# Optimization experiments

Measured on AMD Instinct MI355X. Metric: run time of the kernel, lower is better.

## Reference

```python
import jax, jax.numpy as jnp
import numpy as np
from jax import lax

NUM_CLASSES = 80
TOPK = 13
ALPHA = 1.0
BETA = 6.0
EPS = 1e-9
P = 150000
N = 256


def _make_boxes(key, n, scale):
    k1, k2 = jax.random.split(key)
    xy = jax.random.uniform(k1, (n, 2), dtype=jnp.float32) * scale
    wh = jax.random.uniform(k2, (n, 2), dtype=jnp.float32) * (0.2 * scale) + 1.0
    return jnp.concatenate([xy, xy + wh], axis=-1)  # valid x1y1x2y2


def setup_inputs() -> dict:
    key = jax.random.key(0)
    k1, k2, k3, k4 = jax.random.split(key, 4)
    cls_pred = jax.random.uniform(k1, (P, NUM_CLASSES), dtype=jnp.float32)
    bbox_pred = _make_boxes(k2, P, 640.0)
    bbox_gt = _make_boxes(k3, N, 640.0)
    # FG labels are > 0 (code indexes cls_pred[label-1])
    label_gt = jax.random.randint(k4, (N, 1), 1, NUM_CLASSES + 1, dtype=jnp.int32)
    return {"cls_pred": cls_pred, "bbox_pred": bbox_pred, "label_gt": label_gt, "bbox_gt": bbox_gt}


def _ious(bbox1, bbox2, eps=EPS):
    # bbox1: (N,4) gt, bbox2: (P,4) pred -> (N,P)
    b1 = bbox1[:, None, :]
    b2 = bbox2[None, :, :]
    x1y1 = jnp.maximum(b1[..., 0:2], b2[..., 0:2])
    x2y2 = jnp.minimum(b1[..., 2:4], b2[..., 2:4])
    inter = jnp.clip(x2y2 - x1y1, 0.0).prod(-1)
    area1 = jnp.clip(b1[..., 2:4] - b1[..., 0:2], 0.0).prod(-1)
    area2 = jnp.clip(b2[..., 2:4] - b2[..., 0:2], 0.0).prod(-1)
    return inter / (area1 + area2 - inter + eps)


def _metrics_topk(metrics, topk, eps=EPS):
    n, num_priors = metrics.shape
    topk_vals, topk_idxs = lax.top_k(metrics, topk)  # (N,k)
    keep = topk_vals.max(axis=-1, keepdims=True) > eps
    topk_idxs = jnp.where(keep, topk_idxs, 0)
    rows = jnp.arange(n)[:, None]
    counts = jnp.zeros((n, num_priors), jnp.int32).at[rows, topk_idxs].add(1)
    is_in_topk = jnp.where(counts > 1, 0, counts)
    return is_in_topk.astype(metrics.dtype)


def reference(cls_pred, bbox_pred, label_gt, bbox_gt):
    num_priors, num_classes = cls_pred.shape
    n_gt = bbox_gt.shape[0]
    ious = _ious(bbox_gt, bbox_pred)  # (N,P)
    lbl = label_gt.reshape(-1).astype(jnp.int32)  # (N,)
    bbox_cls_scores = jnp.take(cls_pred.T, lbl - 1, axis=0)  # (N,P)
    alignment_metrics = jnp.power(bbox_cls_scores, ALPHA) * jnp.power(ious, BETA)
    mask_positive = _metrics_topk(alignment_metrics, TOPK)  # (N,P) float 0/1
    mask_positive_sum = mask_positive.sum(axis=0)  # (P,)
    # conflict resolution: priors claimed by >1 gt go to the max-iou gt.
    # Applying unconditionally equals the torch data-dependent branch.
    is_max_iou = (jnp.arange(n_gt)[:, None] == ious.argmax(axis=0)[None, :]).astype(ious.dtype)
    mask_positive = jnp.where(mask_positive_sum[None, :] > 1, is_max_iou, mask_positive)
    mask_positive_sum = mask_positive.sum(axis=0)
    assigned_gt_index = mask_positive.argmax(axis=0)  # (P,)
    assigned_labels = lbl[assigned_gt_index]  # (P,)
    assigned_cls = jax.nn.one_hot(assigned_labels - 1, num_classes, dtype=jnp.int32)
    assigned_bboxes = bbox_gt[assigned_gt_index]  # (P,4)
    assigned_labels = jnp.where(mask_positive_sum > 0, assigned_labels, 0)
    return (assigned_gt_index, assigned_labels, assigned_cls, assigned_bboxes)
```

## Files before the change

### kernel.cpp

```cpp
#include <hip/hip_runtime.h>

#define TOPK 13
#define NCLS 80
#define EPSF 1e-9f
#define NSEG 32
#define GPB  8
#define CAP3 512
#define SEGK 16

typedef unsigned long long u64;

__device__ __forceinline__ u64 shfl_xor64(u64 x, int m) {
    int lo = __shfl_xor((int)(unsigned)(x & 0xFFFFFFFFull), m, 64);
    int hi = __shfl_xor((int)(unsigned)(x >> 32), m, 64);
    return ((u64)(unsigned)hi << 32) | (unsigned)lo;
}

__global__ __launch_bounds__(256) void setup(const int* __restrict__ lbl,
                                             int* __restrict__ count,
                                             int* __restrict__ firstg,
                                             int* __restrict__ gorder, int P, int N) {
    int t = threadIdx.x;
    if (blockIdx.x == 0) {
        __shared__ int key[256];
        key[t] = (t < N) ? ((lbl[t] << 8) | t) : 0x7FFFFFFF;
        __syncthreads();
        for (int k = 2; k <= 256; k <<= 1) {
            for (int j = k >> 1; j >= 1; j >>= 1) {
                int ixj = t ^ j;
                if (ixj > t) {
                    int a = key[t], b = key[ixj];
                    bool up = ((t & k) == 0);
                    if (up ? (a > b) : (a < b)) { key[t] = b; key[ixj] = a; }
                }
                __syncthreads();
            }
        }
        if (t < N) gorder[t] = key[t] & 0xFF;
    } else {
        int base = (blockIdx.x - 1) * 1024 + t * 4;
        if (base + 3 < P) {
            *(int4*)&count[base]  = make_int4(0, 0, 0, 0);
            *(int4*)&firstg[base] = make_int4(0x7FFFFFFF, 0x7FFFFFFF, 0x7FFFFFFF, 0x7FFFFFFF);
        } else {
            for (int i = base; i < P; i++) { count[i] = 0; firstg[i] = 0x7FFFFFFF; }
        }
    }
}

__global__ __launch_bounds__(512, 8) void phaseA1(const float* __restrict__ cls,
                                                  const float4* __restrict__ bboxp,
                                                  const float4* __restrict__ bboxg,
                                                  const int* __restrict__ lbl,
                                                  const int* __restrict__ gorder,
                                                  u64* __restrict__ cand,
                                                  int P, int N, int seglen) {
#pragma clang fp contract(off)
    const int s = blockIdx.x, tile = blockIdx.y, t = threadIdx.x;
    const int wv = t >> 6, lane = t & 63;
    const int pstart = s * seglen;
    int pend = pstart + seglen; if (pend > P) pend = P;

    __shared__ int pbuf[GPB][CAP3];
    __shared__ int ctr[GPB];

    float4 gb[GPB];
#pragma unroll
    for (int j = 0; j < GPB; j++) {
        int gi8 = tile * GPB + j;
        int gj = (gi8 < N) ? gorder[gi8] : -1;
        gb[j] = (gj >= 0) ? bboxg[gj] : make_float4(0.f, 0.f, 0.f, 0.f);
    }
    if (t < GPB) ctr[t] = 0;
    __syncthreads();

    auto testapp = [&](float4 pb, int p, bool force) {
#pragma unroll
        for (int j = 0; j < GPB; j++) {
            float dx = fminf(gb[j].z, pb.z) - fmaxf(gb[j].x, pb.x);
            float dy = fminf(gb[j].w, pb.w) - fmaxf(gb[j].y, pb.y);
            bool want = ((dx > 0.0f) && (dy > 0.0f)) || force;
            if (want) {
                int slot = atomicAdd(&ctr[j], 1);
                if (slot < CAP3) pbuf[j][slot] = p;
            }
        }
    };

    int p = pstart + t;
    if (p < pend) { testapp(bboxp[p], p, t < 16); p += 512; }
    for (; p + 1536 < pend; p += 2048) {
        float4 pb0 = bboxp[p];
        float4 pb1 = bboxp[p + 512];
        float4 pb2 = bboxp[p + 1024];
        float4 pb3 = bboxp[p + 1536];
        testapp(pb0, p, false);
        testapp(pb1, p + 512, false);
        testapp(pb2, p + 1024, false);
        testapp(pb3, p + 1536, false);
    }
    for (; p < pend; p += 512) testapp(bboxp[p], p, false);
    __syncthreads();

    if (wv >= GPB / 2) return;

    const int half = lane >> 5;
    const int l    = lane & 31;
    const int slot = (wv << 1) | half;
    const int gi8 = tile * GPB + slot;
    const bool myValid = gi8 < N;
    const int gj = myValid ? gorder[gi8] : 0;
    const float4 gbw = bboxg[gj];
    const float gaw = fmaxf(gbw.z - gbw.x, 0.0f) * fmaxf(gbw.w - gbw.y, 0.0f);
    const int cidx = lbl[gj] - 1;
    const int rawtotal = ctr[slot];

    u64 K[16];
#pragma unroll
    for (int k = 0; k < 16; k++) K[k] = 0ull;

    auto ins = [&](u64 key) {
        if (key > K[TOPK - 1]) {
#pragma unroll
            for (int k = TOPK - 1; k >= 1; k--) {
                bool a = key > K[k - 1];
                K[k] = a ? K[k - 1] : (key > K[k] ? key : K[k]);
            }
            if (key > K[0]) K[0] = key;
        }
    };

    auto evalk = [&](float4 pb, float sc, int pp) -> u64 {
        float pa = fmaxf(pb.z - pb.x, 0.0f) * fmaxf(pb.w - pb.y, 0.0f);
        float xx1 = fmaxf(gbw.x, pb.x), yy1 = fmaxf(gbw.y, pb.y);
        float xx2 = fminf(gbw.z, pb.z), yy2 = fminf(gbw.w, pb.w);
        float inter = fmaxf(xx2 - xx1, 0.0f) * fmaxf(yy2 - yy1, 0.0f);
        float iou = inter / (((gaw + pa) - inter) + EPSF);
        float i2 = iou * iou;
        float m = sc * ((i2 * i2) * i2);
        unsigned ub = __float_as_uint(m);
        ub ^= ((unsigned)((int)ub >> 31)) | 0x80000000u;
        return ((u64)ub << 32) | (unsigned)(0x7FFFFFFF - pp);
    };

    if (rawtotal <= CAP3) {
        int e = l;
        for (; e + 32 < rawtotal; e += 64) {
            int pp0 = pbuf[slot][e];
            int pp1 = pbuf[slot][e + 32];
            float4 pb0 = bboxp[pp0];
            float4 pb1 = bboxp[pp1];
            float sc0 = cls[(size_t)pp0 * NCLS + cidx];
            float sc1 = cls[(size_t)pp1 * NCLS + cidx];
            u64 k0 = evalk(pb0, sc0, pp0);
            u64 k1 = evalk(pb1, sc1, pp1);
            ins(k0);
            ins(k1);
        }
        for (; e < rawtotal; e += 32) {
            int pp = pbuf[slot][e];
            float4 pb = bboxp[pp];
            float sc = cls[(size_t)pp * NCLS + cidx];
            ins(evalk(pb, sc, pp));
        }
    } else if (myValid) {
        for (int pp = pstart + l; pp < pend; pp += 32) {
            float4 pb = bboxp[pp];
            float sc = cls[(size_t)pp * NCLS + cidx];
            ins(evalk(pb, sc, pp));
        }
    }

    for (int str = 1; str <= 16; str <<= 1) {
#pragma unroll
        for (int i = 0; i < 8; i++) {
            u64 pa = shfl_xor64(K[15 - i], str);
            u64 pb = shfl_xor64(K[i], str);
            u64 a = K[i], b = K[15 - i];
            K[i]      = (a > pa) ? a : pa;
            K[15 - i] = (b > pb) ? b : pb;
        }
        if (str == 16) break;
#pragma unroll
        for (int j = 8; j >= 1; j >>= 1) {
#pragma unroll
            for (int i = 0; i < 16; i++) {
                if ((i & j) == 0) {
                    u64 a = K[i], b = K[i | j];
                    K[i] = (a > b) ? a : b;
                    K[i | j] = (a > b) ? b : a;
                }
            }
        }
    }

    u64 outk = 0ull;
#pragma unroll
    for (int k = 0; k < SEGK; k++) outk = (l == k) ? K[k] : outk;
    if (l < SEGK && myValid)
        cand[((size_t)gj * NSEG + s) * SEGK + l] = outk;
}

__global__ __launch_bounds__(64) void phaseA2(const u64* __restrict__ cand,
                                              int* __restrict__ count,
                                              int* __restrict__ firstg) {
    const int g = blockIdx.x;
    const int lane = threadIdx.x;
    const u64* src = cand + (size_t)g * (NSEG * SEGK);

    u64 K[16];
#pragma unroll
    for (int k = 0; k < 16; k++) K[k] = 0ull;

#pragma unroll
    for (int k = 0; k < (NSEG * SEGK) / 64; k++) {
        u64 key = src[lane + (k << 6)];
        if (key > K[TOPK - 1]) {
#pragma unroll
            for (int q = TOPK - 1; q >= 1; q--) {
                bool a = key > K[q - 1];
                K[q] = a ? K[q - 1] : (key > K[q] ? key : K[q]);
            }
            if (key > K[0]) K[0] = key;
        }
    }

    for (int str = 1; str < 64; str <<= 1) {
#pragma unroll
        for (int i = 0; i < 8; i++) {
            u64 pa = shfl_xor64(K[15 - i], str);
            u64 pb = shfl_xor64(K[i], str);
            u64 a = K[i], b = K[15 - i];
            K[i]      = (a > pa) ? a : pa;
            K[15 - i] = (b > pb) ? b : pb;
        }
#pragma unroll
        for (int j = 8; j >= 1; j >>= 1) {
#pragma unroll
            for (int i = 0; i < 16; i++) {
                if ((i & j) == 0) {
                    u64 a = K[i], b = K[i | j];
                    K[i] = (a > b) ? a : b;
                    K[i | j] = (a > b) ? b : a;
                }
            }
        }
    }

    const unsigned encEpsHi = __float_as_uint(EPSF) | 0x80000000u;
    if (lane < TOPK && (unsigned)(K[0] >> 32) > encEpsHi) {
        u64 outk = 0ull;
#pragma unroll
        for (int k = 0; k < TOPK; k++) outk = (lane == k) ? K[k] : outk;
        int pi = 0x7FFFFFFF - (int)(unsigned)(outk & 0xFFFFFFFFull);
        atomicAdd(&count[pi], 1);
        atomicMin(&firstg[pi], g);
    }
}

__global__ __launch_bounds__(256) void phaseCF(const float4* __restrict__ bboxp,
                                               const float4* __restrict__ bboxg,
                                               const int* __restrict__ lbl,
                                               const int* __restrict__ count,
                                               const int* __restrict__ firstg,
                                               float* __restrict__ out0,
                                               float* __restrict__ out1,
                                               float4* __restrict__ outcls4,
                                               float4* __restrict__ outbox4, int P, int N) {
#pragma clang fp contract(off)
    __shared__ float4 gbS[256];
    __shared__ int glS[256];
    __shared__ int clsl[256];
    int t = threadIdx.x;
    if (t < N) { gbS[t] = bboxg[t]; glS[t] = lbl[t]; }
    __syncthreads();
    int p0 = blockIdx.x * 256;
    int nloc = P - p0; if (nloc > 256) nloc = 256;
    if (t < nloc) {
        int p = p0 + t;
        int cnt = count[p];
        int gi = 0, pos = 0;
        if (cnt == 1) { gi = firstg[p]; pos = 1; }
        else if (cnt > 1) {
            float4 pb = bboxp[p];
            float pa = fmaxf(pb.z - pb.x, 0.0f) * fmaxf(pb.w - pb.y, 0.0f);
            float best = -1.0f;
            for (int g = 0; g < N; g++) {
                float4 g4 = gbS[g];
                float gar = fmaxf(g4.z - g4.x, 0.0f) * fmaxf(g4.w - g4.y, 0.0f);
                float xx1 = fmaxf(g4.x, pb.x), yy1 = fmaxf(g4.y, pb.y);
                float xx2 = fminf(g4.z, pb.z), yy2 = fminf(g4.w, pb.w);
                float inter = fmaxf(xx2 - xx1, 0.0f) * fmaxf(yy2 - yy1, 0.0f);
                float iou = inter / (((gar + pa) - inter) + EPSF);
                if (iou > best) { best = iou; gi = g; }
            }
            pos = 1;
        }
        out0[p] = (float)gi;
        out1[p] = pos ? (float)glS[gi] : 0.0f;
        clsl[t] = glS[gi] - 1;
        outbox4[p] = gbS[gi];
    }
    __syncthreads();
    for (int f = t; f < nloc * 20; f += 256) {
        int pl = f / 20, q = f - pl * 20;
        int cl = clsl[pl], c0 = q * 4;
        float4 vv = make_float4(c0 == cl ? 1.0f : 0.0f, c0 + 1 == cl ? 1.0f : 0.0f,
                                c0 + 2 == cl ? 1.0f : 0.0f, c0 + 3 == cl ? 1.0f : 0.0f);
        outcls4[(size_t)p0 * 20 + f] = vv;
    }
}

__global__ __launch_bounds__(256) void phaseC1(const float4* __restrict__ bboxp,
                                               const float4* __restrict__ bboxg,
                                               const int* __restrict__ lbl,
                                               const int* __restrict__ count,
                                               const int* __restrict__ firstg,
                                               float* __restrict__ out0,
                                               float* __restrict__ out1, int P, int N) {
#pragma clang fp contract(off)
    __shared__ float4 gbS[256];
    __shared__ int glS[256];
    if (threadIdx.x < (unsigned)N) {
        gbS[threadIdx.x] = bboxg[threadIdx.x];
        glS[threadIdx.x] = lbl[threadIdx.x];
    }
    __syncthreads();
    int p = blockIdx.x * 256 + threadIdx.x;
    if (p >= P) return;
    int cnt = count[p];
    int gi = 0, pos = 0;
    if (cnt == 1) { gi = firstg[p]; pos = 1; }
    else if (cnt > 1) {
        float4 pb = bboxp[p];
        float pa = fmaxf(pb.z - pb.x, 0.0f) * fmaxf(pb.w - pb.y, 0.0f);
        float best = -1.0f;
        for (int g = 0; g < N; g++) {
            float4 g4 = gbS[g];
            float gar = fmaxf(g4.z - g4.x, 0.0f) * fmaxf(g4.w - g4.y, 0.0f);
            float xx1 = fmaxf(g4.x, pb.x), yy1 = fmaxf(g4.y, pb.y);
            float xx2 = fminf(g4.z, pb.z), yy2 = fminf(g4.w, pb.w);
            float inter = fmaxf(xx2 - xx1, 0.0f) * fmaxf(yy2 - yy1, 0.0f);
            float iou = inter / (((gar + pa) - inter) + EPSF);
            if (iou > best) { best = iou; gi = g; }
        }
        pos = 1;
    }
    out0[p] = (float)gi;
    out1[p] = pos ? (float)glS[gi] : 0.0f;
}

__global__ __launch_bounds__(256) void phaseC2(const float4* __restrict__ bboxg,
                                               const int* __restrict__ lbl,
                                               const float* __restrict__ out0,
                                               float* __restrict__ outcls,
                                               float* __restrict__ outbox, int P, int N) {
    __shared__ float gbb[256 * 4];
    __shared__ int glS[256];
    __shared__ int clsl[256];
    __shared__ int gil[256];
    int tid = threadIdx.x;
    if (tid < N) {
        float4 b = bboxg[tid];
        gbb[tid * 4 + 0] = b.x; gbb[tid * 4 + 1] = b.y;
        gbb[tid * 4 + 2] = b.z; gbb[tid * 4 + 3] = b.w;
        glS[tid] = lbl[tid];
    }
    __syncthreads();
    int p0 = blockIdx.x * 256;
    int nloc = P - p0; if (nloc > 256) nloc = 256;
    if (tid < nloc) {
        int gi = (int)out0[p0 + tid];
        gil[tid] = gi;
        clsl[tid] = glS[gi] - 1;
    }
    __syncthreads();
    for (int f = tid; f < nloc * NCLS; f += 256) {
        int pl = f / NCLS;
        int c  = f - pl * NCLS;
        outcls[(size_t)p0 * NCLS + f] = (c == clsl[pl]) ? 1.0f : 0.0f;
    }
    for (int f = tid; f < nloc * 4; f += 256) {
        int pl = f >> 2, k = f & 3;
        outbox[(size_t)p0 * 4 + f] = gbb[gil[pl] * 4 + k];
    }
}

extern "C" void kernel_launch(void* const* d_in, const int* in_sizes, int n_in,
                              void* d_out, int out_size, void* d_ws, size_t ws_size,
                              hipStream_t stream) {
    const float* cls_pred  = (const float*)d_in[0];
    const float* bbox_pred = (const float*)d_in[1];
    const int*   label_gt  = (const int*)d_in[2];
    const float* bbox_gt   = (const float*)d_in[3];
    int P = in_sizes[1] / 4;
    int N = in_sizes[3] / 4;

    float* out    = (float*)d_out;
    float* out0   = out;
    float* out1   = out + (size_t)P;
    float* outcls = out + (size_t)2 * P;
    float* outbox = out + (size_t)82 * P;

    int pb = (P + 255) / 256;
    int seglen = (P + NSEG - 1) / NSEG;
    int gtiles = (N + GPB - 1) / GPB;
    dim3 gridA1(NSEG, gtiles);
    int setupBlocks = 1 + (P + 1023) / 1024;
    size_t candBytes = (size_t)N * NSEG * SEGK * sizeof(u64);
    size_t needWs = (size_t)P * 8 + candBytes + (size_t)N * 4 + 64;

    if (ws_size >= needWs) {
        int* count  = (int*)d_ws;
        int* firstg = count + P;
        u64* cand   = (u64*)(firstg + P);
        int* gorder = (int*)((char*)cand + candBytes);

        setup<<<setupBlocks, 256, 0, stream>>>(label_gt, count, firstg, gorder, P, N);
        phaseA1<<<gridA1, 512, 0, stream>>>(cls_pred, (const float4*)bbox_pred,
                                            (const float4*)bbox_gt, label_gt, gorder,
                                            cand, P, N, seglen);
        phaseA2<<<N, 64, 0, stream>>>(cand, count, firstg);
        phaseCF<<<pb, 256, 0, stream>>>((const float4*)bbox_pred, (const float4*)bbox_gt,
                                        label_gt, count, firstg, out0, out1,
                                        (float4*)outcls, (float4*)outbox, P, N);
    } else {
        int* count  = (int*)outbox;
        int* firstg = ((int*)outbox) + P;
        u64* cand   = (u64*)outcls;
        int* gorder = (int*)((char*)cand + candBytes);

        setup<<<setupBlocks, 256, 0, stream>>>(label_gt, count, firstg, gorder, P, N);
        phaseA1<<<gridA1, 512, 0, stream>>>(cls_pred, (const float4*)bbox_pred,
                                            (const float4*)bbox_gt, label_gt, gorder,
                                            cand, P, N, seglen);
        phaseA2<<<N, 64, 0, stream>>>(cand, count, firstg);
        phaseC1<<<pb, 256, 0, stream>>>((const float4*)bbox_pred, (const float4*)bbox_gt,
                                        label_gt, count, firstg, out0, out1, P, N);
        phaseC2<<<pb, 256, 0, stream>>>((const float4*)bbox_gt, label_gt, out0,
                                        outcls, outbox, P, N);
    }
}
```

Baseline: 209.3 us.

## Move per-segment top-k out of phaseA1, write raw candidate keys for phaseA2

phaseA1 now uses one full wavefront per GT, where before two GTs shared a wave at 32 lanes each. Its filtered candidates are scored and written unsorted to a per-(gt,segment) buffer of up to CAP3 keys, with a count array; the in-kernel top-k and bitonic merge only run on the overflow path. phaseA2 grows to 256 threads per GT: each of 4 waves scans 8 segments' candidate lists with insertion top-k, then a 64-key bitonic sort in one wave picks the final 13. This aims to cut phaseA1 register pressure and serial insertion work and to use more lanes, at the cost of a much larger candidate workspace (N*32*512*8 bytes) and more global traffic, which may not fit in the fallback output buffer.

```diff
diff --git a/kernel.cpp b/kernel.cpp
--- a/kernel.cpp
+++ b/kernel.cpp
@@ -6,13 +6,17 @@
 #define NSEG 32
 #define GPB  8
 #define CAP3 512
-#define SEGK 16
 
 typedef unsigned long long u64;
 
 __device__ __forceinline__ u64 shfl_xor64(u64 x, int m) {
     int lo = __shfl_xor((int)(unsigned)(x & 0xFFFFFFFFull), m, 64);
     int hi = __shfl_xor((int)(unsigned)(x >> 32), m, 64);
+    return ((u64)(unsigned)hi << 32) | (unsigned)lo;
+}
+__device__ __forceinline__ u64 shfl64(u64 x, int src) {
+    int lo = __shfl((int)(unsigned)(x & 0xFFFFFFFFull), src, 64);
+    int hi = __shfl((int)(unsigned)(x >> 32), src, 64);
     return ((u64)(unsigned)hi << 32) | (unsigned)lo;
 }
 
@@ -54,6 +58,7 @@
                                                   const int* __restrict__ lbl,
                                                   const int* __restrict__ gorder,
                                                   u64* __restrict__ cand,
+                                                  int* __restrict__ cnt,
                                                   int P, int N, int seglen) {
 #pragma clang fp contract(off)
     const int s = blockIdx.x, tile = blockIdx.y, t = threadIdx.x;
@@ -102,33 +107,14 @@
     for (; p < pend; p += 512) testapp(bboxp[p], p, false);
     __syncthreads();
 
-    if (wv >= GPB / 2) return;
-
-    const int half = lane >> 5;
-    const int l    = lane & 31;
-    const int slot = (wv << 1) | half;
-    const int gi8 = tile * GPB + slot;
-    const bool myValid = gi8 < N;
-    const int gj = myValid ? gorder[gi8] : 0;
+    const int gi8 = tile * GPB + wv;
+    if (gi8 >= N) return;
+    const int gj = gorder[gi8];
     const float4 gbw = bboxg[gj];
     const float gaw = fmaxf(gbw.z - gbw.x, 0.0f) * fmaxf(gbw.w - gbw.y, 0.0f);
     const int cidx = lbl[gj] - 1;
-    const int rawtotal = ctr[slot];
-
-    u64 K[16];
-#pragma unroll
-    for (int k = 0; k < 16; k++) K[k] = 0ull;
-
-    auto ins = [&](u64 key) {
-        if (key > K[TOPK - 1]) {
-#pragma unroll
-            for (int k = TOPK - 1; k >= 1; k--) {
-                bool a = key > K[k - 1];
-                K[k] = a ? K[k - 1] : (key > K[k] ? key : K[k]);
-            }
-            if (key > K[0]) K[0] = key;
-        }
-    };
+    const int rawtotal = ctr[wv];
+    u64* outp = cand + ((size_t)gj * NSEG + s) * CAP3;
 
     auto evalk = [&](float4 pb, float sc, int pp) -> u64 {
         float pa = fmaxf(pb.z - pb.x, 0.0f) * fmaxf(pb.w - pb.y, 0.0f);
@@ -144,34 +130,111 @@
     };
 
     if (rawtotal <= CAP3) {
-        int e = l;
-        for (; e + 32 < rawtotal; e += 64) {
-            int pp0 = pbuf[slot][e];
-            int pp1 = pbuf[slot][e + 32];
+        if (lane == 0) cnt[gj * NSEG + s] = rawtotal;
+        int e = lane;
+        for (; e + 64 < rawtotal; e += 128) {
+            int pp0 = pbuf[wv][e];
+            int pp1 = pbuf[wv][e + 64];
             float4 pb0 = bboxp[pp0];
             float4 pb1 = bboxp[pp1];
             float sc0 = cls[(size_t)pp0 * NCLS + cidx];
             float sc1 = cls[(size_t)pp1 * NCLS + cidx];
-            u64 k0 = evalk(pb0, sc0, pp0);
-            u64 k1 = evalk(pb1, sc1, pp1);
-            ins(k0);
-            ins(k1);
-        }
-        for (; e < rawtotal; e += 32) {
-            int pp = pbuf[slot][e];
+            outp[e]      = evalk(pb0, sc0, pp0);
+            outp[e + 64] = evalk(pb1, sc1, pp1);
+        }
+        for (; e < rawtotal; e += 64) {
+            int pp = pbuf[wv][e];
+            outp[e] = evalk(bboxp[pp], cls[(size_t)pp * NCLS + cidx], pp);
+        }
+    } else {
+        u64 K[16];
+#pragma unroll
+        for (int k = 0; k < 16; k++) K[k] = 0ull;
+        auto ins = [&](u64 key) {
+            if (key > K[TOPK - 1]) {
+#pragma unroll
+                for (int k = TOPK - 1; k >= 1; k--) {
+                    bool a = key > K[k - 1];
+                    K[k] = a ? K[k - 1] : (key > K[k] ? key : K[k]);
+                }
+                if (key > K[0]) K[0] = key;
+            }
+        };
+        for (int pp = pstart + lane; pp < pend; pp += 64) {
             float4 pb = bboxp[pp];
             float sc = cls[(size_t)pp * NCLS + cidx];
             ins(evalk(pb, sc, pp));
         }
-    } else if (myValid) {
-        for (int pp = pstart + l; pp < pend; pp += 32) {
-            float4 pb = bboxp[pp];
-            float sc = cls[(size_t)pp * NCLS + cidx];
-            ins(evalk(pb, sc, pp));
-        }
-    }
-
-    for (int str = 1; str <= 16; str <<= 1) {
+        for (int str = 1; str <= 32; str <<= 1) {
+#pragma unroll
+            for (int i = 0; i < 8; i++) {
+                u64 pa = shfl_xor64(K[15 - i], str);
+                u64 pb = shfl_xor64(K[i], str);
+                u64 a = K[i], b = K[15 - i];
+                K[i]      = (a > pa) ? a : pa;
+                K[15 - i] = (b > pb) ? b : pb;
+            }
+            if (str == 32) break;
+#pragma unroll
+            for (int j = 8; j >= 1; j >>= 1) {
+#pragma unroll
+                for (int i = 0; i < 16; i++) {
+                    if ((i & j) == 0) {
+                        u64 a = K[i], b = K[i | j];
+                        K[i] = (a > b) ? a : b;
+                        K[i | j] = (a > b) ? b : a;
+                    }
+                }
+            }
+        }
+        u64 outk = 0ull;
+#pragma unroll
+        for (int k = 0; k < 16; k++) outk = (lane == k) ? K[k] : outk;
+        if (lane < 16) outp[lane] = outk;
+        if (lane == 0) cnt[gj * NSEG + s] = 16;
+    }
+}
+
+__global__ __launch_bounds__(256) void phaseA2(const u64* __restrict__ cand,
+                                               const int* __restrict__ cnt,
+                                               int* __restrict__ count,
+                                               int* __restrict__ firstg) {
+    const int g = blockIdx.x;
+    const int w = threadIdx.x >> 6, lane = threadIdx.x & 63;
+    __shared__ u64 sk[64];
+
+    u64 K[16];
+#pragma unroll
+    for (int k = 0; k < 16; k++) K[k] = 0ull;
+
+    auto ins = [&](u64 key) {
+        if (key > K[TOPK - 1]) {
+#pragma unroll
+            for (int q = TOPK - 1; q >= 1; q--) {
+                bool a = key > K[q - 1];
+                K[q] = a ? K[q - 1] : (key > K[q] ? key : K[q]);
+            }
+            if (key > K[0]) K[0] = key;
+        }
+    };
+
+    const u64* base = cand + (size_t)g * (NSEG * CAP3);
+    const int* cb = cnt + g * NSEG;
+    for (int s8 = 0; s8 < NSEG / 4; s8++) {
+        int sseg = w * (NSEG / 4) + s8;
+        int m = cb[sseg];
+        const u64* sp = base + (size_t)sseg * CAP3;
+        int e = lane;
+        for (; e + 64 < m; e += 128) {
+            u64 k0 = sp[e];
+            u64 k1 = sp[e + 64];
+            ins(k0);
+            ins(k1);
+        }
+        for (; e < m; e += 64) ins(sp[e]);
+    }
+
+    for (int str = 1; str <= 32; str <<= 1) {
 #pragma unroll
         for (int i = 0; i < 8; i++) {
             u64 pa = shfl_xor64(K[15 - i], str);
@@ -180,7 +243,7 @@
             K[i]      = (a > pa) ? a : pa;
             K[15 - i] = (b > pb) ? b : pb;
         }
-        if (str == 16) break;
+        if (str == 32) break;
 #pragma unroll
         for (int j = 8; j >= 1; j >>= 1) {
 #pragma unroll
@@ -193,68 +256,31 @@
             }
         }
     }
-
     u64 outk = 0ull;
 #pragma unroll
-    for (int k = 0; k < SEGK; k++) outk = (l == k) ? K[k] : outk;
-    if (l < SEGK && myValid)
-        cand[((size_t)gj * NSEG + s) * SEGK + l] = outk;
-}
-
-__global__ __launch_bounds__(64) void phaseA2(const u64* __restrict__ cand,
-                                              int* __restrict__ count,
-                                              int* __restrict__ firstg) {
-    const int g = blockIdx.x;
-    const int lane = threadIdx.x;
-    const u64* src = cand + (size_t)g * (NSEG * SEGK);
-
-    u64 K[16];
-#pragma unroll
-    for (int k = 0; k < 16; k++) K[k] = 0ull;
-
-#pragma unroll
-    for (int k = 0; k < (NSEG * SEGK) / 64; k++) {
-        u64 key = src[lane + (k << 6)];
-        if (key > K[TOPK - 1]) {
-#pragma unroll
-            for (int q = TOPK - 1; q >= 1; q--) {
-                bool a = key > K[q - 1];
-                K[q] = a ? K[q - 1] : (key > K[q] ? key : K[q]);
-            }
-            if (key > K[0]) K[0] = key;
-        }
-    }
-
-    for (int str = 1; str < 64; str <<= 1) {
-#pragma unroll
-        for (int i = 0; i < 8; i++) {
-            u64 pa = shfl_xor64(K[15 - i], str);
-            u64 pb = shfl_xor64(K[i], str);
-            u64 a = K[i], b = K[15 - i];
-            K[i]      = (a > pa) ? a : pa;
-            K[15 - i] = (b > pb) ? b : pb;
-        }
-#pragma unroll
-        for (int j = 8; j >= 1; j >>= 1) {
-#pragma unroll
-            for (int i = 0; i < 16; i++) {
-                if ((i & j) == 0) {
-                    u64 a = K[i], b = K[i | j];
-                    K[i] = (a > b) ? a : b;
-                    K[i | j] = (a > b) ? b : a;
-                }
-            }
-        }
-    }
-
-    const unsigned encEpsHi = __float_as_uint(EPSF) | 0x80000000u;
-    if (lane < TOPK && (unsigned)(K[0] >> 32) > encEpsHi) {
-        u64 outk = 0ull;
-#pragma unroll
-        for (int k = 0; k < TOPK; k++) outk = (lane == k) ? K[k] : outk;
-        int pi = 0x7FFFFFFF - (int)(unsigned)(outk & 0xFFFFFFFFull);
-        atomicAdd(&count[pi], 1);
-        atomicMin(&firstg[pi], g);
+    for (int k = 0; k < 16; k++) outk = (lane == k) ? K[k] : outk;
+    if (lane < 16) sk[w * 16 + lane] = outk;
+    __syncthreads();
+
+    if (w == 0) {
+        u64 key = sk[lane];
+        for (int k = 2; k <= 64; k <<= 1) {
+            for (int j = k >> 1; j >= 1; j >>= 1) {
+                u64 pk = shfl_xor64(key, j);
+                bool lower = (lane & j) == 0;
+                bool desc  = (lane & k) == 0;
+                bool keepmax = (lower == desc);
+                bool pgt = pk > key;
+                key = (keepmax == pgt) ? pk : key;
+            }
+        }
+        u64 mx = shfl64(key, 0);
+        const unsigned encEpsHi = __float_as_uint(EPSF) | 0x80000000u;
+        if (lane < TOPK && (unsigned)(mx >> 32) > encEpsHi) {
+            int pi = 0x7FFFFFFF - (int)(unsigned)(key & 0xFFFFFFFFull);
+            atomicAdd(&count[pi], 1);
+            atomicMin(&firstg[pi], g);
+        }
     }
 }
 
@@ -278,10 +304,10 @@
     int nloc = P - p0; if (nloc > 256) nloc = 256;
     if (t < nloc) {
         int p = p0 + t;
-        int cnt = count[p];
+        int cnt_ = count[p];
         int gi = 0, pos = 0;
-        if (cnt == 1) { gi = firstg[p]; pos = 1; }
-        else if (cnt > 1) {
+        if (cnt_ == 1) { gi = firstg[p]; pos = 1; }
+        else if (cnt_ > 1) {
             float4 pb = bboxp[p];
             float pa = fmaxf(pb.z - pb.x, 0.0f) * fmaxf(pb.w - pb.y, 0.0f);
             float best = -1.0f;
@@ -328,10 +354,10 @@
     __syncthreads();
     int p = blockIdx.x * 256 + threadIdx.x;
     if (p >= P) return;
-    int cnt = count[p];
+    int cnt_ = count[p];
     int gi = 0, pos = 0;
-    if (cnt == 1) { gi = firstg[p]; pos = 1; }
-    else if (cnt > 1) {
+    if (cnt_ == 1) { gi = firstg[p]; pos = 1; }
+    else if (cnt_ > 1) {
         float4 pb = bboxp[p];
         float pa = fmaxf(pb.z - pb.x, 0.0f) * fmaxf(pb.w - pb.y, 0.0f);
         float best = -1.0f;
@@ -407,20 +433,22 @@
     int gtiles = (N + GPB - 1) / GPB;
     dim3 gridA1(NSEG, gtiles);
     int setupBlocks = 1 + (P + 1023) / 1024;
-    size_t candBytes = (size_t)N * NSEG * SEGK * sizeof(u64);
-    size_t needWs = (size_t)P * 8 + candBytes + (size_t)N * 4 + 64;
+    size_t candBytes = (size_t)N * NSEG * CAP3 * sizeof(u64);
+    size_t cntBytes  = (size_t)N * NSEG * sizeof(int);
+    size_t needWs = (size_t)P * 8 + candBytes + cntBytes + (size_t)N * 4 + 64;
 
     if (ws_size >= needWs) {
         int* count  = (int*)d_ws;
         int* firstg = count + P;
         u64* cand   = (u64*)(firstg + P);
-        int* gorder = (int*)((char*)cand + candBytes);
+        int* cnt    = (int*)((char*)cand + candBytes);
+        int* gorder = cnt + (size_t)N * NSEG;
 
         setup<<<setupBlocks, 256, 0, stream>>>(label_gt, count, firstg, gorder, P, N);
         phaseA1<<<gridA1, 512, 0, stream>>>(cls_pred, (const float4*)bbox_pred,
                                             (const float4*)bbox_gt, label_gt, gorder,
-                                            cand, P, N, seglen);
-        phaseA2<<<N, 64, 0, stream>>>(cand, count, firstg);
+                                            cand, cnt, P, N, seglen);
+        phaseA2<<<N, 256, 0, stream>>>(cand, cnt, count, firstg);
         phaseCF<<<pb, 256, 0, stream>>>((const float4*)bbox_pred, (const float4*)bbox_gt,
                                         label_gt, count, firstg, out0, out1,
                                         (float4*)outcls, (float4*)outbox, P, N);
@@ -428,13 +456,14 @@
         int* count  = (int*)outbox;
         int* firstg = ((int*)outbox) + P;
         u64* cand   = (u64*)outcls;
-        int* gorder = (int*)((char*)cand + candBytes);
+        int* cnt    = (int*)((char*)cand + candBytes);
+        int* gorder = cnt + (size_t)N * NSEG;
 
         setup<<<setupBlocks, 256, 0, stream>>>(label_gt, count, firstg, gorder, P, N);
         phaseA1<<<gridA1, 512, 0, stream>>>(cls_pred, (const float4*)bbox_pred,
                                             (const float4*)bbox_gt, label_gt, gorder,
-                                            cand, P, N, seglen);
-        phaseA2<<<N, 64, 0, stream>>>(cand, count, firstg);
+                                            cand, cnt, P, N, seglen);
+        phaseA2<<<N, 256, 0, stream>>>(cand, cnt, count, firstg);
         phaseC1<<<pb, 256, 0, stream>>>((const float4*)bbox_pred, (const float4*)bbox_gt,
                                         label_gt, count, firstg, out0, out1, P, N);
         phaseC2<<<pb, 256, 0, stream>>>((const float4*)bbox_gt, label_gt, out0,
```

New measurement: 212.5 us. Within noise of the previous version (+1.5%).
